# Optimization experiments

Measured on AMD Instinct MI355X. Metric: run time of the kernel, lower is better.

## Reference

```python
import jax, jax.numpy as jnp
import numpy as np

N = 51200      # total nodes
G = 256        # graphs in batch
NPG = 200      # nodes per graph
E = 409600     # intra-graph edges
EPG = E // G
F_IN, HID, HEADS, NCLS = 768, 128, 4, 2


def setup_inputs() -> dict:
    key = jax.random.key(0)
    ks = jax.random.split(key, 20)
    x = jax.random.normal(ks[0], (N, F_IN), jnp.float32)
    # edges strictly inside each graph, no self-loops (PyG batching semantics)
    gid = jnp.arange(E, dtype=jnp.int32) // EPG
    sl = jax.random.randint(ks[1], (E,), 0, NPG, dtype=jnp.int32)
    off = jax.random.randint(ks[2], (E,), 1, NPG, dtype=jnp.int32)
    dl = (sl + off) % NPG
    edge_index = jnp.stack([gid * NPG + sl, gid * NPG + dl])
    batch = jnp.arange(N, dtype=jnp.int32) // NPG

    def glorot(k, shape, fan_in):
        return jax.random.normal(k, shape, jnp.float32) * np.float32(1.0 / np.sqrt(fan_in))

    return {
        'x': x, 'edge_index': edge_index, 'batch': batch,
        'W1': glorot(ks[3], (F_IN, HEADS * HID), F_IN),
        'a_src1': glorot(ks[4], (HEADS, HID), HID),
        'a_dst1': glorot(ks[5], (HEADS, HID), HID),
        'b1': jnp.zeros((HEADS * HID,), jnp.float32),
        'W2': glorot(ks[6], (HEADS * HID, HID), HEADS * HID),
        'a_src2': glorot(ks[7], (1, HID), HID),
        'a_dst2': glorot(ks[8], (1, HID), HID),
        'b2': jnp.zeros((HID,), jnp.float32),
        'Wc': glorot(ks[9], (HID, 2), HID),
        'bc': jnp.zeros((2,), jnp.float32),
        'Wf1': glorot(ks[10], (HID, HID), HID),
        'bf1': jnp.zeros((HID,), jnp.float32),
        'Wf2': glorot(ks[11], (HID, NCLS), HID),
        'bf2': jnp.zeros((NCLS,), jnp.float32),
    }


def _segment_softmax(logits, seg, num):
    m = jax.ops.segment_max(logits, seg, num_segments=num)
    e = jnp.exp(logits - m[seg])
    s = jax.ops.segment_sum(e, seg, num_segments=num)
    return e / (s[seg] + 1e-16)


def _gat(x, src, dst, W, a_s, a_d, b, n):
    # PyG GATConv, eval mode (attention dropout off), self-loops already in src/dst
    H, C = a_s.shape
    h = (x @ W).reshape(n, H, C)                       # [n,H,C]
    a_src = (h * a_s).sum(-1)                          # [n,H]
    a_dst = (h * a_d).sum(-1)
    logits = jax.nn.leaky_relu(a_src[src] + a_dst[dst], 0.2)  # [Etot,H]
    alpha = _segment_softmax(logits, dst, n)
    out = jax.ops.segment_sum(h[src] * alpha[:, :, None], dst, num_segments=n)
    return out.reshape(n, H * C) + b


def reference(x, edge_index, batch, W1, a_src1, a_dst1, b1, W2, a_src2, a_dst2, b2,
              Wc, bc, Wf1, bf1, Wf2, bf2):
    src0, dst0 = edge_index[0], edge_index[1]
    loop = jnp.arange(N, dtype=src0.dtype)
    src = jnp.concatenate([src0, loop])
    dst = jnp.concatenate([dst0, loop])

    h1 = jax.nn.relu(_gat(x, src, dst, W1, a_src1, a_dst1, b1, N))     # [N,512]
    h2 = jax.nn.relu(_gat(h1, src, dst, W2, a_src2, a_dst2, b2, N))    # [N,128]

    S = jax.nn.softmax(h2 @ Wc + bc, axis=1)                           # [N,2]

    # aggregate(): per-graph S^T A S via per-edge outer products (A from original edges)
    eg = batch[src0]
    outer = S[src0][:, :, None] * S[dst0][:, None, :]                  # [E,2,2]
    agg = jax.ops.segment_sum(outer, eg, num_segments=G)               # [G,2,2]
    rnorm = jnp.clip(jnp.abs(agg).sum(axis=2, keepdims=True), 1e-5, None)  # F.normalize p=1 dim=1
    nadj = agg / rnorm
    diag = jnp.diagonal(nadj, axis1=1, axis2=2)                        # [G,2]
    aggregate_loss = jnp.mean(jnp.mean((diag - 1.0) ** 2, axis=1))     # MSE vs ones, averaged over graphs

    # subgraph embedding: first row of S_g^T x_g per graph
    sub = jax.ops.segment_sum(S[:, 0:1] * h2, batch, num_segments=G)   # [G,128]

    out = jax.nn.relu(sub @ Wf1 + bf1)                                 # eval: dropout off
    out = out @ Wf2 + bf2                                              # [G,2]
    return out, aggregate_loss
```

## Files before the change

### kernel.cpp

```cpp
#include <hip/hip_runtime.h>
#include <hip/hip_bf16.h>
#include <cstdint>

#define N_NODES 51200
#define N_GRAPH 256
#define NPG     200
#define N_EDGE  409600
#define EPG     1600
#define F_IN    768
#define HID     128
#define HEADS   4
#define HC      512

typedef __attribute__((ext_vector_type(8))) short short8;
typedef __attribute__((ext_vector_type(4))) float floatx4;

constexpr size_t OFF_H1B    = 0;
constexpr size_t OFF_H2B    = OFF_H1B + (size_t)N_NODES * HC * 2;
constexpr size_t OFF_H2F    = OFF_H2B + (size_t)N_NODES * HID * 2;
constexpr size_t OFF_WT1    = OFF_H2F + (size_t)N_NODES * HID * 4;
constexpr size_t OFF_WT2    = OFF_WT1 + (size_t)HC * F_IN * 2;
constexpr size_t OFF_S      = OFF_WT2 + (size_t)HID * HC * 2;
constexpr size_t OFF_AGG    = OFF_S + (size_t)N_NODES * 2 * 4;
constexpr size_t OFF_SUB    = OFF_AGG + (size_t)N_GRAPH * 4 * 4;
constexpr size_t OFF_EORD   = OFF_SUB + (size_t)N_GRAPH * HID * 4;
constexpr size_t OFF_ROWS   = OFF_EORD + (size_t)N_GRAPH * EPG * 2;

__device__ __forceinline__ float leaky(float x) { return x >= 0.0f ? x : 0.2f * x; }

__device__ __forceinline__ unsigned short f2bf(float f) {
    unsigned int u = __float_as_uint(f);
    u += 0x7fffu + ((u >> 16) & 1u);
    return (unsigned short)(u >> 16);
}
__device__ __forceinline__ float bflo(int p) { return __uint_as_float((unsigned)p << 16); }
__device__ __forceinline__ float bfhi(int p) { return __uint_as_float((unsigned)p & 0xffff0000u); }

__device__ __forceinline__ int   fmono(float x) { int u = __float_as_int(x); return u ^ ((u >> 31) | 0x80000000); }
__device__ __forceinline__ float imono(int k)   { int u = k ^ (((~k) >> 31) | 0x80000000); return __int_as_float(u); }

__device__ __forceinline__ unsigned int cvtpk(float lo, float hi) {
    unsigned int r;
    asm("v_cvt_pk_bf16_f32 %0, %1, %2" : "=v"(r) : "v"(lo), "v"(hi));
    return r;
}

__device__ __forceinline__ void gl_lds16(const void* g, void* l) {
    __builtin_amdgcn_global_load_lds(
        (__attribute__((address_space(1))) void*)(g),
        (__attribute__((address_space(3))) void*)(l),
        16, 0, 0);
}

__global__ __launch_bounds__(256)
void transpose_cvt_kernel(const float* __restrict__ W, short* __restrict__ Wt,
                          int K, int Nn)
{
    int idx = blockIdx.x * 256 + threadIdx.x;
    if (idx >= K * Nn) return;
    int k = idx / Nn, n = idx % Nn;
    Wt[(size_t)n * K + k] = (short)f2bf(W[idx]);
}

__global__ __launch_bounds__(512, 4)
void gemm_xw1_kernel(const float* __restrict__ A, const short* __restrict__ Bt,
                     unsigned short* __restrict__ C, int M, int Nn, int K)
{
    __shared__ __align__(16) float Asm[2][128 * 32];
    __shared__ __align__(16) short Bsm[2][256 * 32];
    const int tid = threadIdx.x;
    const int w = tid >> 6, l = tid & 63;

    const int nwg = gridDim.x;
    int wg = blockIdx.x;
    wg = (wg & 7) * (nwg >> 3) + (wg >> 3);
    const int nbx = Nn >> 8;
    const int m0 = (wg / nbx) * 128;
    const int n0 = (wg % nbx) * 256;
    const int wr = w >> 2, wc = w & 3;

    floatx4 acc[4][4];
#pragma unroll
    for (int i = 0; i < 4; ++i)
#pragma unroll
        for (int j = 0; j < 4; ++j) acc[i][j] = (floatx4)0.0f;

    const short* bgp = Bt + (size_t)(n0 + w * 32 + (l & 15)) * K + ((l >> 4) * 8);
    const float* agp = A + (size_t)(m0 + w * 16 + (l & 7)) * K + ((l >> 3) * 4);
    const int nt = K >> 5;

    int aB[4];
#pragma unroll
    for (int mi = 0; mi < 4; ++mi) {
        const int r = wr * 64 + mi * 16 + (l & 15);
        aB[mi] = (r >> 3) * 256 + (l >> 4) * 64 + (r & 7) * 4;
    }
    const int bB0 = wc * 2048 + l * 8;

#define STAGEX(buf, t) {                                                        \
        const int ko_ = (t) * 32;                                               \
        gl_lds16(agp + ko_,              &Asm[buf][w * 512]);                   \
        gl_lds16(agp + 8 * K + ko_,      &Asm[buf][w * 512 + 256]);             \
        gl_lds16(bgp + ko_,              &Bsm[buf][w * 1024]);                  \
        gl_lds16(bgp + 16 * K + ko_,     &Bsm[buf][w * 1024 + 512]); }

#define COMPUTEX(buf) {                                                         \
        short8 af[4], bfr[4];                                                   \
        _Pragma("unroll")                                                       \
        for (int mi = 0; mi < 4; ++mi) {                                        \
            float4 v0 = *(const float4*)&Asm[buf][aB[mi]];                      \
            float4 v1 = *(const float4*)&Asm[buf][aB[mi] + 32];                 \
            uint4 pk;                                                           \
            pk.x = cvtpk(v0.x, v0.y); pk.y = cvtpk(v0.z, v0.w);                 \
            pk.z = cvtpk(v1.x, v1.y); pk.w = cvtpk(v1.z, v1.w);                 \
            af[mi] = *reinterpret_cast<short8*>(&pk);                           \
        }                                                                       \
        _Pragma("unroll")                                                       \
        for (int ni = 0; ni < 4; ++ni)                                          \
            bfr[ni] = *(const short8*)&Bsm[buf][bB0 + ni * 512];                \
        _Pragma("unroll")                                                       \
        for (int mi = 0; mi < 4; ++mi)                                          \
            _Pragma("unroll")                                                   \
            for (int ni = 0; ni < 4; ++ni)                                      \
                acc[mi][ni] = __builtin_amdgcn_mfma_f32_16x16x32_bf16(          \
                    af[mi], bfr[ni], acc[mi][ni], 0, 0, 0); }

    STAGEX(0, 0);
    __syncthreads();

    int cur = 0;
    for (int t = 0; t < nt; ++t) {
        if (t + 1 < nt) STAGEX(cur ^ 1, t + 1);
        COMPUTEX(cur);
        __syncthreads();
        cur ^= 1;
    }
#undef STAGEX
#undef COMPUTEX

    const int lr = (l >> 4) * 4, lc = l & 15;
#pragma unroll
    for (int mi = 0; mi < 4; ++mi)
#pragma unroll
        for (int ni = 0; ni < 4; ++ni) {
            const size_t base = (size_t)(m0 + wr * 64 + mi * 16 + lr) * Nn
                              + (n0 + wc * 64 + ni * 16 + lc);
#pragma unroll
            for (int rr = 0; rr < 4; ++rr)
                C[base + (size_t)rr * Nn] = f2bf(acc[mi][ni][rr]);
        }
}

__global__ __launch_bounds__(256)
void gemm_bf16_kernel(const short* __restrict__ Ab, const short* __restrict__ Bt,
                      unsigned short* __restrict__ C, int M, int Nn, int K)
{
    __shared__ __align__(16) short Bblob[3][4096];
    __shared__ __align__(16) short Ablob[3][4096];
    const int tid = threadIdx.x;
    const int w = tid >> 6, l = tid & 63;

    const int nwg = gridDim.x;
    int wg = blockIdx.x;
    wg = (wg & 7) * (nwg >> 3) + (wg >> 3);
    const int nbx = Nn >> 7;
    const int m0 = (wg / nbx) * 128;
    const int n0 = (wg % nbx) * 128;
    const int wr = w >> 1, wc = w & 1;
    const int wofs = w * 1024;

    floatx4 acc[4][4];
#pragma unroll
    for (int i = 0; i < 4; ++i)
#pragma unroll
        for (int j = 0; j < 4; ++j) acc[i][j] = (floatx4)0.0f;

    const short* bgp = Bt + (size_t)(n0 + w * 32 + (l & 15)) * K + ((l >> 4) * 8);
    const short* agp = Ab + (size_t)(m0 + w * 32 + (l & 15)) * K + ((l >> 4) * 8);
    const int nt = K >> 5;

    auto compute = [&](int bi) {
        short8 af[4], bfr[4];
#pragma unroll
        for (int mi = 0; mi < 4; ++mi)
            af[mi] = *(const short8*)&Ablob[bi][(wr * 4 + mi) * 512 + l * 8];
#pragma unroll
        for (int ni = 0; ni < 4; ++ni)
            bfr[ni] = *(const short8*)&Bblob[bi][(wc * 4 + ni) * 512 + l * 8];
#pragma unroll
        for (int mi = 0; mi < 4; ++mi)
#pragma unroll
            for (int ni = 0; ni < 4; ++ni)
                acc[mi][ni] = __builtin_amdgcn_mfma_f32_16x16x32_bf16(
                    af[mi], bfr[ni], acc[mi][ni], 0, 0, 0);
    };

    gl_lds16(agp,               &Ablob[0][wofs]);
    gl_lds16(agp + 16 * K,      &Ablob[0][wofs + 512]);
    gl_lds16(bgp,               &Bblob[0][wofs]);
    gl_lds16(bgp + 16 * K,      &Bblob[0][wofs + 512]);
    gl_lds16(agp + 32,          &Ablob[1][wofs]);
    gl_lds16(agp + 16 * K + 32, &Ablob[1][wofs + 512]);
    gl_lds16(bgp + 32,          &Bblob[1][wofs]);
    gl_lds16(bgp + 16 * K + 32, &Bblob[1][wofs + 512]);
    asm volatile("s_waitcnt vmcnt(4)" ::: "memory");
    __builtin_amdgcn_s_barrier();

    int cur3 = 0;
    for (int t = 0; t < nt; ++t) {
        int nn3 = cur3 + 2; if (nn3 >= 3) nn3 -= 3;
        if (t + 2 < nt) {
            const int kk = (t + 2) << 5;
            gl_lds16(agp + kk,          &Ablob[nn3][wofs]);
            gl_lds16(agp + 16 * K + kk, &Ablob[nn3][wofs + 512]);
            gl_lds16(bgp + kk,          &Bblob[nn3][wofs]);
            gl_lds16(bgp + 16 * K + kk, &Bblob[nn3][wofs + 512]);
        }
        compute(cur3);
        if (t + 1 < nt) {
            if (t + 2 < nt) asm volatile("s_waitcnt vmcnt(4) lgkmcnt(0)" ::: "memory");
            else            asm volatile("s_waitcnt vmcnt(0) lgkmcnt(0)" ::: "memory");
            __builtin_amdgcn_s_barrier();
        }
        cur3 += 1; if (cur3 == 3) cur3 = 0;
    }

    const int lr = (l >> 4) * 4, lc = l & 15;
#pragma unroll
    for (int mi = 0; mi < 4; ++mi)
#pragma unroll
        for (int ni = 0; ni < 4; ++ni) {
            const size_t base = (size_t)(m0 + wr * 64 + mi * 16 + lr) * Nn
                              + (n0 + wc * 64 + ni * 16 + lc);
#pragma unroll
            for (int rr = 0; rr < 4; ++rr)
                C[base + (size_t)rr * Nn] = f2bf(acc[mi][ni][rr]);
        }
}

__global__ __launch_bounds__(256)
void csr_kernel(const int* __restrict__ src0, const int* __restrict__ dst0,
                unsigned short* __restrict__ eord, int* __restrict__ rows)
{
    const int g = blockIdx.x, tid = threadIdx.x;
    __shared__ unsigned short s_eraw[EPG];
    __shared__ int s_cnt[NPG];
    __shared__ int s_scan[256];
    __shared__ int s_row[NPG + 1];
    const int gbase = g * NPG;

    if (tid < NPG) s_cnt[tid] = 0;
    for (int j = tid; j < EPG; j += 256) {
        int s = src0[g * EPG + j] - gbase;
        int d = dst0[g * EPG + j] - gbase;
        s_eraw[j] = (unsigned short)(s | (d << 8));
    }
    __syncthreads();
    for (int j = tid; j < EPG; j += 256)
        atomicAdd(&s_cnt[s_eraw[j] >> 8], 1);
    __syncthreads();
    {
        int v = (tid < NPG) ? s_cnt[tid] : 0;
        s_scan[tid] = v;
        __syncthreads();
        for (int off = 1; off < 256; off <<= 1) {
            int u = (tid >= off) ? s_scan[tid - off] : 0;
            __syncthreads();
            s_scan[tid] += u;
            __syncthreads();
        }
        if (tid < NPG) s_row[tid + 1] = s_scan[tid];
        if (tid == 0) s_row[0] = 0;
        __syncthreads();
        if (tid < NPG) s_scan[tid] = s_row[tid];
    }
    __syncthreads();
    for (int j = tid; j < EPG; j += 256) {
        int pk = s_eraw[j];
        int p = atomicAdd(&s_scan[pk >> 8], 1);
        eord[(size_t)g * EPG + p] = (unsigned short)pk;
    }
    if (tid <= NPG) rows[g * (NPG + 1) + tid] = s_row[tid];
}

__global__ __launch_bounds__(512)
void gat1_kernel(const unsigned short* __restrict__ H,
                 const unsigned short* __restrict__ eord, const int* __restrict__ rows,
                 const float* __restrict__ a_s, const float* __restrict__ a_d,
                 const float* __restrict__ b1, unsigned short* __restrict__ out)
{
    const int g = blockIdx.x, h = blockIdx.y;
    __shared__ int   s_feat[NPG * 64];
    __shared__ float s_as[NPG], s_ad[NPG], s_m[NPG], s_sum[NPG];
    __shared__ int   s_mi[NPG];
    __shared__ int   s_row[NPG + 1];
    __shared__ int2  s_wc[EPG];
    const int tid = threadIdx.x, w = tid >> 6, l = tid & 63;
    const int gbase = g * NPG;

    for (int c = 0; c < 7; ++c) {
        const int base = c * 512 + w * 64;
        if (base < NPG * 16) {
            const int flat = base + l;
            const int row = flat >> 4, q = flat & 15;
            gl_lds16(H + (size_t)(gbase + row) * HC + h * HID + q * 8,
                     &s_feat[base * 4]);
        }
    }
    for (int j = tid; j < EPG; j += 512)
        s_wc[j].y = eord[(size_t)g * EPG + j];
    if (tid <= NPG) s_row[tid] = rows[g * (NPG + 1) + tid];
    __syncthreads();

    const float2 av = ((const float2*)(a_s + h * HID))[l];
    const float2 dv = ((const float2*)(a_d + h * HID))[l];
    for (int nl = w; nl < NPG; nl += 8) {
        int pk = s_feat[nl * 64 + l];
        float f0 = bflo(pk), f1 = bfhi(pk);
        float ss = f0 * av.x + f1 * av.y;
        float sd = f0 * dv.x + f1 * dv.y;
#pragma unroll
        for (int off = 1; off < 64; off <<= 1) {
            ss += __shfl_xor(ss, off);
            sd += __shfl_xor(sd, off);
        }
        if (l == 0) {
            s_as[nl] = ss; s_ad[nl] = sd;
            s_mi[nl] = fmono(leaky(ss + sd));
        }
    }
    __syncthreads();

    for (int j = tid; j < EPG; j += 512) {
        int pk = s_wc[j].y;
        float lg = leaky(s_as[pk & 255] + s_ad[pk >> 8]);
        s_wc[j].x = __float_as_int(lg);
        atomicMax(&s_mi[pk >> 8], fmono(lg));
    }
    __syncthreads();

    if (tid < NPG) {
        float m = imono(s_mi[tid]);
        s_m[tid] = m;
        s_sum[tid] = __expf(leaky(s_as[tid] + s_ad[tid]) - m);
    }
    __syncthreads();

    for (int j = tid; j < EPG; j += 512) {
        int2 e = s_wc[j];
        float ev = __expf(__int_as_float(e.x) - s_m[e.y >> 8]);
        s_wc[j].x = __float_as_int(ev);
        atomicAdd(&s_sum[e.y >> 8], ev);
    }
    __syncthreads();

    const float2 bv = ((const float2*)(b1 + h * HID))[l];
    for (int nl = w; nl < NPG; nl += 8) {
        const int r0 = s_row[nl], r1 = s_row[nl + 1];
        const float wself = __expf(leaky(s_as[nl] + s_ad[nl]) - s_m[nl]);
        int spk = s_feat[nl * 64 + l];
        float a0 = wself * bflo(spk), a1 = wself * bfhi(spk);
        float c0 = 0.0f, c1 = 0.0f;
        int j = r0;
        for (; j + 4 <= r1; j += 4) {
            int2 e0 = s_wc[j], e1 = s_wc[j + 1], e2 = s_wc[j + 2], e3 = s_wc[j + 3];
            int p0 = s_feat[(e0.y & 255) * 64 + l];
            int p1 = s_feat[(e1.y & 255) * 64 + l];
            int p2 = s_feat[(e2.y & 255) * 64 + l];
            int p3 = s_feat[(e3.y & 255) * 64 + l];
            float w0 = __int_as_float(e0.x), w1 = __int_as_float(e1.x);
            float w2 = __int_as_float(e2.x), w3 = __int_as_float(e3.x);
            a0 += w0 * bflo(p0); a1 += w0 * bfhi(p0);
            c0 += w1 * bflo(p1); c1 += w1 * bfhi(p1);
            a0 += w2 * bflo(p2); a1 += w2 * bfhi(p2);
            c0 += w3 * bflo(p3); c1 += w3 * bfhi(p3);
        }
        for (; j < r1; ++j) {
            int2 e0 = s_wc[j];
            int p0 = s_feat[(e0.y & 255) * 64 + l];
            float w0 = __int_as_float(e0.x);
            a0 += w0 * bflo(p0); a1 += w0 * bfhi(p0);
        }
        const float inv = 1.0f / (s_sum[nl] + 1e-16f);
        float o0 = (a0 + c0) * inv + bv.x;
        float o1 = (a1 + c1) * inv + bv.y;
        unsigned int st = (unsigned int)f2bf(fmaxf(o0, 0.0f))
                        | ((unsigned int)f2bf(fmaxf(o1, 0.0f)) << 16);
        *(unsigned int*)&out[(size_t)(gbase + nl) * HC + h * HID + 2 * l] = st;
    }
}

__global__ __launch_bounds__(512)
void gat2_kernel(const unsigned short* __restrict__ H,
                 const unsigned short* __restrict__ eord, const int* __restrict__ rows,
                 const float* __restrict__ a_s, const float* __restrict__ a_d,
                 const float* __restrict__ b2, const float* __restrict__ Wc,
                 const float* __restrict__ bc,
                 float* __restrict__ sub, float* __restrict__ agg)
{
    const int g = blockIdx.x;
    __shared__ int   s_feat[NPG * 64];
    __shared__ float s_as[NPG], s_ad[NPG], s_m[NPG], s_sum[NPG];
    __shared__ int   s_mi[NPG];
    __shared__ int   s_row[NPG + 1];
    __shared__ int2  s_wc[EPG];
    __shared__ float2 s_Sv[NPG];
    __shared__ float  s_red[8 * 128];
    __shared__ float  s_aggr[8][4];
    const int tid = threadIdx.x, w = tid >> 6, l = tid & 63;
    const int gbase = g * NPG;

    for (int c = 0; c < 7; ++c) {
        const int base = c * 512 + w * 64;
        if (base < NPG * 16)
            gl_lds16(H + (size_t)gbase * HID + (size_t)(base + l) * 8,
                     &s_feat[base * 4]);
    }
    for (int j = tid; j < EPG; j += 512)
        s_wc[j].y = eord[(size_t)g * EPG + j];
    if (tid <= NPG) s_row[tid] = rows[g * (NPG + 1) + tid];
    __syncthreads();

    const float2 av = ((const float2*)a_s)[l];
    const float2 dv = ((const float2*)a_d)[l];
    for (int nl = w; nl < NPG; nl += 8) {
        int pk = s_feat[nl * 64 + l];
        float f0 = bflo(pk), f1 = bfhi(pk);
        float ss = f0 * av.x + f1 * av.y;
        float sd = f0 * dv.x + f1 * dv.y;
#pragma unroll
        for (int off = 1; off < 64; off <<= 1) {
            ss += __shfl_xor(ss, off);
            sd += __shfl_xor(sd, off);
        }
        if (l == 0) {
            s_as[nl] = ss; s_ad[nl] = sd;
            s_mi[nl] = fmono(leaky(ss + sd));
        }
    }
    __syncthreads();

    for (int j = tid; j < EPG; j += 512) {
        int pk = s_wc[j].y;
        float lg = leaky(s_as[pk & 255] + s_ad[pk >> 8]);
        s_wc[j].x = __float_as_int(lg);
        atomicMax(&s_mi[pk >> 8], fmono(lg));
    }
    __syncthreads();

    if (tid < NPG) {
        float m = imono(s_mi[tid]);
        s_m[tid] = m;
        s_sum[tid] = __expf(leaky(s_as[tid] + s_ad[tid]) - m);
    }
    __syncthreads();

    for (int j = tid; j < EPG; j += 512) {
        int2 e = s_wc[j];
        float ev = __expf(__int_as_float(e.x) - s_m[e.y >> 8]);
        s_wc[j].x = __float_as_int(ev);
        atomicAdd(&s_sum[e.y >> 8], ev);
    }
    __syncthreads();

    const float2 bv = ((const float2*)b2)[l];
    const float4 wcv = ((const float4*)Wc)[l];
    const float bc0 = bc[0], bc1 = bc[1];
    float accs0 = 0.0f, accs1 = 0.0f;
    for (int nl = w; nl < NPG; nl += 8) {
        const int r0 = s_row[nl], r1 = s_row[nl + 1];
        const float wself = __expf(leaky(s_as[nl] + s_ad[nl]) - s_m[nl]);
        int spk = s_feat[nl * 64 + l];
        float a0 = wself * bflo(spk), a1 = wself * bfhi(spk);
        float c0 = 0.0f, c1 = 0.0f;
        int j = r0;
        for (; j + 4 <= r1; j += 4) {
            int2 e0 = s_wc[j], e1 = s_wc[j + 1], e2 = s_wc[j + 2], e3 = s_wc[j + 3];
            int p0 = s_feat[(e0.y & 255) * 64 + l];
            int p1 = s_feat[(e1.y & 255) * 64 + l];
            int p2 = s_feat[(e2.y & 255) * 64 + l];
            int p3 = s_feat[(e3.y & 255) * 64 + l];
            float w0 = __int_as_float(e0.x), w1 = __int_as_float(e1.x);
            float w2 = __int_as_float(e2.x), w3 = __int_as_float(e3.x);
            a0 += w0 * bflo(p0); a1 += w0 * bfhi(p0);
            c0 += w1 * bflo(p1); c1 += w1 * bfhi(p1);
            a0 += w2 * bflo(p2); a1 += w2 * bfhi(p2);
            c0 += w3 * bflo(p3); c1 += w3 * bfhi(p3);
        }
        for (; j < r1; ++j) {
            int2 e0 = s_wc[j];
            int p0 = s_feat[(e0.y & 255) * 64 + l];
            float w0 = __int_as_float(e0.x);
            a0 += w0 * bflo(p0); a1 += w0 * bfhi(p0);
        }
        const float inv = 1.0f / (s_sum[nl] + 1e-16f);
        float o0 = fmaxf((a0 + c0) * inv + bv.x, 0.0f);
        float o1 = fmaxf((a1 + c1) * inv + bv.y, 0.0f);
        float z0 = o0 * wcv.x + o1 * wcv.z;
        float z1 = o0 * wcv.y + o1 * wcv.w;
#pragma unroll
        for (int off = 1; off < 64; off <<= 1) {
            z0 += __shfl_xor(z0, off);
            z1 += __shfl_xor(z1, off);
        }
        z0 += bc0; z1 += bc1;
        float mm = fmaxf(z0, z1);
        float e0 = __expf(z0 - mm), e1 = __expf(z1 - mm);
        float is = 1.0f / (e0 + e1);
        float s0v = e0 * is, s1v = e1 * is;
        if (l == 0) s_Sv[nl] = make_float2(s0v, s1v);
        accs0 += s0v * o0;
        accs1 += s0v * o1;
    }
    s_red[w * 128 + 2 * l]     = accs0;
    s_red[w * 128 + 2 * l + 1] = accs1;
    __syncthreads();

    float a00 = 0, a01 = 0, a10 = 0, a11 = 0;
    for (int j = tid; j < EPG; j += 512) {
        int pk = s_wc[j].y;
        float2 Ss = s_Sv[pk & 255];
        float2 Sd = s_Sv[pk >> 8];
        a00 += Ss.x * Sd.x; a01 += Ss.x * Sd.y;
        a10 += Ss.y * Sd.x; a11 += Ss.y * Sd.y;
    }
#pragma unroll
    for (int off = 32; off > 0; off >>= 1) {
        a00 += __shfl_down(a00, off); a01 += __shfl_down(a01, off);
        a10 += __shfl_down(a10, off); a11 += __shfl_down(a11, off);
    }
    if (l == 0) { s_aggr[w][0] = a00; s_aggr[w][1] = a01; s_aggr[w][2] = a10; s_aggr[w][3] = a11; }
    __syncthreads();

    if (tid < 128) {
        float s = 0.0f;
#pragma unroll
        for (int w8 = 0; w8 < 8; ++w8) s += s_red[w8 * 128 + tid];
        sub[(size_t)g * HID + tid] = s;
    }
    if (tid < 4) {
        float s = 0.0f;
#pragma unroll
        for (int w8 = 0; w8 < 8; ++w8) s += s_aggr[w8][tid];
        agg[g * 4 + tid] = s;
    }
}

__global__ __launch_bounds__(256)
void loss_kernel(const float* __restrict__ agg, float* __restrict__ out_loss)
{
    int tid = threadIdx.x;
    float a00 = agg[tid*4 + 0], a01 = agg[tid*4 + 1];
    float a10 = agg[tid*4 + 2], a11 = agg[tid*4 + 3];
    float rn0 = fmaxf(fabsf(a00) + fabsf(a01), 1e-5f);
    float rn1 = fmaxf(fabsf(a10) + fabsf(a11), 1e-5f);
    float d0 = a00 / rn0 - 1.0f, d1 = a11 / rn1 - 1.0f;
    float contrib = 0.5f * (d0*d0 + d1*d1);
    for (int off = 32; off > 0; off >>= 1) contrib += __shfl_down(contrib, off);
    __shared__ float sred[4];
    if ((tid & 63) == 0) sred[tid >> 6] = contrib;
    __syncthreads();
    if (tid == 0)
        out_loss[0] = (sred[0] + sred[1] + sred[2] + sred[3]) * (1.0f / N_GRAPH);
}

__global__ __launch_bounds__(128)
void final_kernel(const float* __restrict__ sub, const float* __restrict__ Wf1,
                  const float* __restrict__ bf1, const float* __restrict__ Wf2,
                  const float* __restrict__ bf2, float* __restrict__ out)
{
    __shared__ float s_sub[128];
    __shared__ float s_fc[128];
    const int g = blockIdx.x, t = threadIdx.x;
    s_sub[t] = sub[g*HID + t];
    __syncthreads();
    float acc = bf1[t];
    for (int c = 0; c < 128; ++c)
        acc += s_sub[c] * Wf1[c*128 + t];
    s_fc[t] = fmaxf(acc, 0.0f);
    __syncthreads();
    if (t < 2) {
        float z = bf2[t];
        for (int j = 0; j < 128; ++j) z += s_fc[j] * Wf2[j*2 + t];
        out[g*2 + t] = z;
    }
}

extern "C" void kernel_launch(void* const* d_in, const int* in_sizes, int n_in,
                              void* d_out, int out_size, void* d_ws, size_t ws_size,
                              hipStream_t stream)
{
    const float* x   = (const float*)d_in[0];
    const int*   ei  = (const int*)d_in[1];
    const float* W1  = (const float*)d_in[3];
    const float* as1 = (const float*)d_in[4];
    const float* ad1 = (const float*)d_in[5];
    const float* b1  = (const float*)d_in[6];
    const float* W2  = (const float*)d_in[7];
    const float* as2 = (const float*)d_in[8];
    const float* ad2 = (const float*)d_in[9];
    const float* b2  = (const float*)d_in[10];
    const float* Wc  = (const float*)d_in[11];
    const float* bc  = (const float*)d_in[12];
    const float* Wf1 = (const float*)d_in[13];
    const float* bf1 = (const float*)d_in[14];
    const float* Wf2 = (const float*)d_in[15];
    const float* bf2 = (const float*)d_in[16];
    const int* src0 = ei;
    const int* dst0 = ei + N_EDGE;

    char* ws = (char*)d_ws;
    unsigned short* H1b = (unsigned short*)(ws + OFF_H1B);
    unsigned short* H2b = (unsigned short*)(ws + OFF_H2B);
    short* Wt1   = (short*)(ws + OFF_WT1);
    short* Wt2   = (short*)(ws + OFF_WT2);
    float* aggb  = (float*)(ws + OFF_AGG);
    float* subb  = (float*)(ws + OFF_SUB);
    unsigned short* eord = (unsigned short*)(ws + OFF_EORD);
    int*   rowsb = (int*)(ws + OFF_ROWS);
    float* out   = (float*)d_out;

    transpose_cvt_kernel<<<(F_IN*HC + 255)/256, 256, 0, stream>>>(W1, Wt1, F_IN, HC);
    transpose_cvt_kernel<<<(HC*HID + 255)/256, 256, 0, stream>>>(W2, Wt2, HC, HID);
    csr_kernel<<<N_GRAPH, 256, 0, stream>>>(src0, dst0, eord, rowsb);

    gemm_xw1_kernel<<<(N_NODES/128) * (HC/256), 512, 0, stream>>>(
        x, Wt1, H1b, N_NODES, HC, F_IN);

    gat1_kernel<<<dim3(N_GRAPH, HEADS), 512, 0, stream>>>(
        H1b, eord, rowsb, as1, ad1, b1, H1b);

    gemm_bf16_kernel<<<(N_NODES/128) * (HID/128), 256, 0, stream>>>(
        (const short*)H1b, Wt2, H2b, N_NODES, HID, HC);

    gat2_kernel<<<N_GRAPH, 512, 0, stream>>>(
        H2b, eord, rowsb, as2, ad2, b2, Wc, bc, subb, aggb);

    loss_kernel<<<1, 256, 0, stream>>>(aggb, out + N_GRAPH*2);
    final_kernel<<<N_GRAPH, 128, 0, stream>>>(subb, Wf1, bf1, Wf2, bf2, out);

    (void)in_sizes; (void)n_in; (void)out_size; (void)ws_size;
}
```

Measured before the change: 509.0 us.

## Triple-buffer B tiles and use fine-grained vmcnt waits in first GEMM

```diff
diff --git a/kernel.cpp b/kernel.cpp
--- a/kernel.cpp
+++ b/kernel.cpp
@@ -62,12 +62,12 @@
     Wt[(size_t)n * K + k] = (short)f2bf(W[idx]);
 }
 
-__global__ __launch_bounds__(512, 4)
+__global__ __launch_bounds__(512, 2)
 void gemm_xw1_kernel(const float* __restrict__ A, const short* __restrict__ Bt,
                      unsigned short* __restrict__ C, int M, int Nn, int K)
 {
     __shared__ __align__(16) float Asm[2][128 * 32];
-    __shared__ __align__(16) short Bsm[2][256 * 32];
+    __shared__ __align__(16) short Bsm[3][256 * 32];
     const int tid = threadIdx.x;
     const int w = tid >> 6, l = tid & 63;
 
@@ -97,19 +97,22 @@
     }
     const int bB0 = wc * 2048 + l * 8;
 
-#define STAGEX(buf, t) {                                                        \
+#define STAGE_A(buf, t) {                                                       \
         const int ko_ = (t) * 32;                                               \
         gl_lds16(agp + ko_,              &Asm[buf][w * 512]);                   \
-        gl_lds16(agp + 8 * K + ko_,      &Asm[buf][w * 512 + 256]);             \
+        gl_lds16(agp + 8 * K + ko_,      &Asm[buf][w * 512 + 256]); }
+
+#define STAGE_B(buf, t) {                                                       \
+        const int ko_ = (t) * 32;                                               \
         gl_lds16(bgp + ko_,              &Bsm[buf][w * 1024]);                  \
         gl_lds16(bgp + 16 * K + ko_,     &Bsm[buf][w * 1024 + 512]); }
 
-#define COMPUTEX(buf) {                                                         \
+#define COMPUTEX(abuf, bbuf) {                                                  \
         short8 af[4], bfr[4];                                                   \
         _Pragma("unroll")                                                       \
         for (int mi = 0; mi < 4; ++mi) {                                        \
-            float4 v0 = *(const float4*)&Asm[buf][aB[mi]];                      \
-            float4 v1 = *(const float4*)&Asm[buf][aB[mi] + 32];                 \
+            float4 v0 = *(const float4*)&Asm[abuf][aB[mi]];                     \
+            float4 v1 = *(const float4*)&Asm[abuf][aB[mi] + 32];                \
             uint4 pk;                                                           \
             pk.x = cvtpk(v0.x, v0.y); pk.y = cvtpk(v0.z, v0.w);                 \
             pk.z = cvtpk(v1.x, v1.y); pk.w = cvtpk(v1.z, v1.w);                 \
@@ -117,7 +120,7 @@
         }                                                                       \
         _Pragma("unroll")                                                       \
         for (int ni = 0; ni < 4; ++ni)                                          \
-            bfr[ni] = *(const short8*)&Bsm[buf][bB0 + ni * 512];                \
+            bfr[ni] = *(const short8*)&Bsm[bbuf][bB0 + ni * 512];               \
         _Pragma("unroll")                                                       \
         for (int mi = 0; mi < 4; ++mi)                                          \
             _Pragma("unroll")                                                   \
@@ -125,17 +128,27 @@
                 acc[mi][ni] = __builtin_amdgcn_mfma_f32_16x16x32_bf16(          \
                     af[mi], bfr[ni], acc[mi][ni], 0, 0, 0); }
 
-    STAGEX(0, 0);
-    __syncthreads();
-
-    int cur = 0;
+    STAGE_B(0, 0);
+    STAGE_A(0, 0);
+    STAGE_B(1, 1);
+    asm volatile("s_waitcnt vmcnt(2)" ::: "memory");
+    __builtin_amdgcn_s_barrier();
+
+    int b3 = 0;
     for (int t = 0; t < nt; ++t) {
-        if (t + 1 < nt) STAGEX(cur ^ 1, t + 1);
-        COMPUTEX(cur);
-        __syncthreads();
-        cur ^= 1;
-    }
-#undef STAGEX
+        if (t + 1 < nt) STAGE_A((t + 1) & 1, t + 1);
+        int bn3 = b3 + 2; if (bn3 >= 3) bn3 -= 3;
+        if (t + 2 < nt) STAGE_B(bn3, t + 2);
+        COMPUTEX(t & 1, b3);
+        if (t + 1 < nt) {
+            if (t + 2 < nt) asm volatile("s_waitcnt vmcnt(2) lgkmcnt(0)" ::: "memory");
+            else            asm volatile("s_waitcnt vmcnt(0) lgkmcnt(0)" ::: "memory");
+            __builtin_amdgcn_s_barrier();
+        }
+        b3 += 1; if (b3 == 3) b3 = 0;
+    }
+#undef STAGE_A
+#undef STAGE_B
 #undef COMPUTEX
 
     const int lr = (l >> 4) * 4, lc = l & 15;
```

New measurement: 507.0 us. About the same (-0.4%).
